# Performance work log

Hardware: AMD Instinct MI355X
Metric: run time of the kernel (lower is better)

Reference implementation:

```python
import jax, jax.numpy as jnp
import numpy as np

B, T_SEQ, STATE, DIM_IN, DIM_K, DIM_V, LAYER = 8, 2048, 128, 1024, 64, 64, 4
T = T_SEQ + 2 * STATE  # 2304
LAMBDA_INIT = 0.8 - 0.6 * float(np.exp(-0.3 * LAYER))
NEG = -1e30


def setup_inputs() -> dict:
    key = jax.random.key(0)
    ks = jax.random.split(key, 20)
    def w(k, shape):
        return jax.random.normal(k, shape, dtype=jnp.float32) * 0.02
    inp = {"x": jax.random.normal(ks[0], (B, T, DIM_IN), dtype=jnp.float32)}
    # projection weights stored as (in, out) so y = x @ W
    inp["Wq"] = w(ks[1], (DIM_IN, 2 * DIM_K)); inp["Wk"] = w(ks[2], (DIM_IN, 2 * DIM_K)); inp["Wv"] = w(ks[3], (DIM_IN, 2 * DIM_V))
    inp["Wq_ss"] = w(ks[4], (DIM_IN, 2 * DIM_K)); inp["Wk_ss"] = w(ks[5], (DIM_IN, 2 * DIM_K)); inp["Wv_ss"] = w(ks[6], (DIM_IN, 2 * DIM_V))
    inp["Wq_se"] = w(ks[7], (DIM_IN, 2 * DIM_K)); inp["Wk_se"] = w(ks[8], (DIM_IN, 2 * DIM_K)); inp["Wv_se"] = w(ks[9], (DIM_IN, 2 * DIM_V))
    # layernorm params (torch defaults: ones/zeros)
    inp["g_in"] = jnp.ones((DIM_IN,), jnp.float32); inp["b_in"] = jnp.zeros((DIM_IN,), jnp.float32)
    inp["g_ss"] = jnp.ones((DIM_IN,), jnp.float32); inp["b_ss"] = jnp.zeros((DIM_IN,), jnp.float32)
    inp["g_se"] = jnp.ones((DIM_IN,), jnp.float32); inp["b_se"] = jnp.zeros((DIM_IN,), jnp.float32)
    inp["g_out"] = jnp.ones((2 * DIM_V,), jnp.float32); inp["b_out"] = jnp.zeros((2 * DIM_V,), jnp.float32)
    # lambda gate params
    inp["lq1"] = jax.random.normal(ks[10], (1, DIM_K), jnp.float32)
    inp["lq2"] = jax.random.normal(ks[11], (1, DIM_K), jnp.float32)
    inp["lk1"] = jax.random.normal(ks[12], (DIM_K, 1), jnp.float32)
    inp["lk2"] = jax.random.normal(ks[13], (DIM_K, 1), jnp.float32)
    return inp


def _ln(z, g, b, eps=1e-5):
    m = jnp.mean(z, axis=-1, keepdims=True)
    v = jnp.mean((z - m) ** 2, axis=-1, keepdims=True)
    return (z - m) * jax.lax.rsqrt(v + eps) * g + b


def reference(x, Wq, Wk, Wv, Wq_ss, Wk_ss, Wv_ss, Wq_se, Wk_se, Wv_se,
              g_in, b_in, g_ss, b_ss, g_se, b_se, g_out, b_out,
              lq1, lq2, lk1, lk2):
    # extract_state: split off state tokens at both ends
    xs, xm, xe = x[:, :STATE], x[:, STATE:-STATE], x[:, -STATE:]
    xm = _ln(xm, g_in, b_in)
    xs = _ln(xs, g_ss, b_ss)
    xe = _ln(xe, g_se, b_se)
    q = jnp.concatenate([xs @ Wq_ss, xm @ Wq, xe @ Wq_se], axis=1)  # (B,T,2K)
    k = jnp.concatenate([xs @ Wk_ss, xm @ Wk, xe @ Wk_se], axis=1)
    v = jnp.concatenate([xs @ Wv_ss, xm @ Wv, xe @ Wv_se], axis=1)  # (B,T,2V)
    q1, q2 = q[..., :DIM_K], q[..., DIM_K:]
    k1, k2 = k[..., :DIM_K], k[..., DIM_K:]
    scale = 1.0 / np.sqrt(DIM_K)
    t = q.shape[1]
    causal = jnp.triu(jnp.full((t, t), NEG, dtype=q.dtype), k=1)  # (T,T)
    s1 = jnp.einsum('btd,bsd->bts', q1, k1) * scale + causal
    s2 = jnp.einsum('btd,bsd->bts', q2, k2) * scale + causal
    a1 = jax.nn.softmax(s1, axis=-1)
    a2 = jax.nn.softmax(s2, axis=-1)
    o1 = jnp.einsum('bts,bsd->btd', a1, v)
    o2 = jnp.einsum('bts,bsd->btd', a2, v)
    lam = (jnp.exp(lq1 @ lk1) - jnp.exp(lq2 @ lk2))[0, 0] + LAMBDA_INIT
    att = o1 - lam * o2
    return _ln(att, g_out, b_out)
```

## Files before the change

kernel.cpp:

```cpp
#include <hip/hip_runtime.h>
#include <hip/hip_bf16.h>
#include <stdint.h>

#define B_ 8
#define T_ 2304
#define DIN 1024
#define LAMBDA_INIT_F 0.6192834728526788f

typedef __bf16 bf16x8 __attribute__((ext_vector_type(8)));
typedef float f32x4 __attribute__((ext_vector_type(4)));

__device__ __forceinline__ unsigned short f2bf(float f) {
    union { float f; unsigned int u; } v; v.f = f;
    unsigned int u = v.u;
    unsigned int r = (u + 0x7FFFu + ((u >> 16) & 1u)) >> 16;
    return (unsigned short)r;
}

__device__ __forceinline__ unsigned int pack2bf(float lo, float hi) {
    return ((unsigned int)f2bf(hi) << 16) | (unsigned int)f2bf(lo);
}

__device__ __forceinline__ float bf2f(unsigned short u) {
    union { unsigned int u; float f; } v; v.u = ((unsigned int)u) << 16;
    return v.f;
}

__device__ __forceinline__ void gload16(const void* g, void* l) {
    __builtin_amdgcn_global_load_lds(
        (const __attribute__((address_space(1))) unsigned int*)g,
        (__attribute__((address_space(3))) unsigned int*)l,
        16, 0, 0);
}

__global__ __launch_bounds__(256) void k_wtrans(
    const float* w0, const float* w1, const float* w2,
    const float* w3, const float* w4, const float* w5,
    const float* w6, const float* w7, const float* w8,
    unsigned short* __restrict__ wt)
{
    __shared__ float tile[64][65];
    int bx = blockIdx.x;
    int mat = bx >> 5;
    int tl = bx & 31;
    int tx = tl & 15;
    int ty = tl >> 4;
    const float* srcs[9] = {w0, w1, w2, w3, w4, w5, w6, w7, w8};
    const float* src = srcs[mat];
    int k0 = tx * 64, c0 = ty * 64;
    int t = threadIdx.x;
    int r = t >> 2, cg = (t & 3) << 4;
    const float* p = src + (size_t)(k0 + r) * 128 + c0 + cg;
#pragma unroll
    for (int i = 0; i < 4; ++i) {
        float4 v = *(const float4*)(p + i * 4);
        tile[r][cg + i * 4 + 0] = v.x;
        tile[r][cg + i * 4 + 1] = v.y;
        tile[r][cg + i * 4 + 2] = v.z;
        tile[r][cg + i * 4 + 3] = v.w;
    }
    __syncthreads();
    int seg = mat / 3, m = mat % 3;
    int crow = seg * 384 + m * 128 + c0 + r;
    unsigned short* dst = wt + (size_t)crow * 1024 + k0 + cg;
    __align__(16) unsigned short ob[16];
#pragma unroll
    for (int i = 0; i < 16; ++i) ob[i] = f2bf(tile[cg + i][r]);
    *(uint4*)(dst) = *(const uint4*)(ob);
    *(uint4*)(dst + 8) = *(const uint4*)(ob + 8);
}

__global__ __launch_bounds__(256) void k_ln(
    const float* __restrict__ x,
    const float* __restrict__ g_in, const float* __restrict__ b_in,
    const float* __restrict__ g_ss, const float* __restrict__ b_ss,
    const float* __restrict__ g_se, const float* __restrict__ b_se,
    unsigned short* __restrict__ xbf)
{
    int row = (blockIdx.x << 2) + (threadIdx.x >> 6);
    int l = threadIdx.x & 63;
    int t = row % T_;
    const float* gv; const float* bv;
    if (t < 128)       { gv = g_ss; bv = b_ss; }
    else if (t < 2176) { gv = g_in; bv = b_in; }
    else               { gv = g_se; bv = b_se; }
    const float* xp = x + (size_t)row * DIN + l * 4;
    float4 v0 = *(const float4*)(xp);
    float4 v1 = *(const float4*)(xp + 256);
    float4 v2 = *(const float4*)(xp + 512);
    float4 v3 = *(const float4*)(xp + 768);
    float s  = v0.x + v0.y + v0.z + v0.w + v1.x + v1.y + v1.z + v1.w
             + v2.x + v2.y + v2.z + v2.w + v3.x + v3.y + v3.z + v3.w;
    float s2 = v0.x*v0.x + v0.y*v0.y + v0.z*v0.z + v0.w*v0.w
             + v1.x*v1.x + v1.y*v1.y + v1.z*v1.z + v1.w*v1.w
             + v2.x*v2.x + v2.y*v2.y + v2.z*v2.z + v2.w*v2.w
             + v3.x*v3.x + v3.y*v3.y + v3.z*v3.z + v3.w*v3.w;
#pragma unroll
    for (int off = 1; off <= 32; off <<= 1) {
        s  += __shfl_xor(s,  off);
        s2 += __shfl_xor(s2, off);
    }
    float mean = s * (1.f / 1024.f);
    float rstd = rsqrtf(s2 * (1.f / 1024.f) - mean * mean + 1e-5f);
    unsigned short* op = xbf + (size_t)row * DIN + l * 4;
    const float* gp = gv + l * 4;
    const float* bp = bv + l * 4;
#pragma unroll
    for (int k = 0; k < 4; ++k) {
        float4 vv = (k == 0) ? v0 : (k == 1) ? v1 : (k == 2) ? v2 : v3;
        float4 gk = *(const float4*)(gp + k * 256);
        float4 bk = *(const float4*)(bp + k * 256);
        uint2 o;
        o.x = pack2bf((vv.x - mean) * rstd * gk.x + bk.x,
                      (vv.y - mean) * rstd * gk.y + bk.y);
        o.y = pack2bf((vv.z - mean) * rstd * gk.z + bk.z,
                      (vv.w - mean) * rstd * gk.w + bk.w);
        *(uint2*)(op + k * 256) = o;
    }
}

__global__ __launch_bounds__(512, 4) void k_proj2(
    const unsigned short* __restrict__ xbf,
    const unsigned short* __restrict__ wt,
    unsigned short* __restrict__ qo,
    unsigned short* __restrict__ ko,
    unsigned short* __restrict__ vto)
{
    __shared__ __align__(16) char smem[81920];

    int bid = blockIdx.x;
    int mt = bid >> 1, ch = bid & 1;
    int bb = mt / 18, tt = mt % 18;
    int seg = (tt == 0) ? 0 : ((tt < 17) ? 1 : 2);
    size_t arow0 = (size_t)mt * 128;
    int ncol0 = ch * 192;
    int wrow0 = seg * 384 + ncol0;

    int tid = threadIdx.x;
    int w = tid >> 6, l = tid & 63;
    int wr = w >> 2, wc = w & 3;
    int g4 = l >> 4, cr = l & 15;

    int rA0 = tid >> 3, cS = (tid & 7) << 4;
    const char* srcA0 = (const char*)xbf + (arow0 + rA0) * 2048 + cS;
    const char* srcA1 = srcA0 + (size_t)64 * 2048;
    int dA0 = rA0 * 128 + (cS ^ ((rA0 & 7) << 4));
    int dA1 = dA0 + 64 * 128;
    const char* srcW0 = (const char*)wt + (size_t)(wrow0 + rA0) * 2048 + cS;
    const char* srcW1 = srcW0 + (size_t)64 * 2048;
    const char* srcW2 = srcW0 + (size_t)128 * 2048;
    int dW0 = dA0, dW1 = dA0 + 64 * 128, dW2 = dA0 + 128 * 128;

    {
        uint4 a0 = *(const uint4*)srcA0;
        uint4 a1 = *(const uint4*)srcA1;
        uint4 w0 = *(const uint4*)srcW0;
        uint4 w1 = *(const uint4*)srcW1;
        uint4 w2 = *(const uint4*)srcW2;
        *(uint4*)(smem + dA0) = a0;
        *(uint4*)(smem + dA1) = a1;
        *(uint4*)(smem + 32768 + dW0) = w0;
        *(uint4*)(smem + 32768 + dW1) = w1;
        *(uint4*)(smem + 32768 + dW2) = w2;
    }
    __syncthreads();

    f32x4 acc[4][3] = {};
    for (int ks = 0; ks < 16; ++ks) {
        bool pf = (ks < 15);
        uint4 pa0, pa1, pw0, pw1, pw2;
        if (pf) {
            size_t o = (size_t)(ks + 1) * 128;
            pa0 = *(const uint4*)(srcA0 + o);
            pa1 = *(const uint4*)(srcA1 + o);
            pw0 = *(const uint4*)(srcW0 + o);
            pw1 = *(const uint4*)(srcW1 + o);
            pw2 = *(const uint4*)(srcW2 + o);
        }
        const char* Ab = smem + (ks & 1) * 16384;
        const char* Wb = smem + 32768 + (ks & 1) * 24576;
        __builtin_amdgcn_s_setprio(1);
#pragma unroll
        for (int kk = 0; kk < 2; ++kk) {
            int kb = kk * 64 + g4 * 16;
            bf16x8 af[4];
#pragma unroll
            for (int r4 = 0; r4 < 4; ++r4) {
                int rr = wr * 64 + r4 * 16 + cr;
                af[r4] = *(const bf16x8*)(Ab + rr * 128 + (kb ^ ((rr & 7) << 4)));
            }
            bf16x8 bfr[3];
#pragma unroll
            for (int nt = 0; nt < 3; ++nt) {
                int c = wc * 48 + nt * 16 + cr;
                bfr[nt] = *(const bf16x8*)(Wb + c * 128 + (kb ^ ((c & 7) << 4)));
            }
#pragma unroll
            for (int r4 = 0; r4 < 4; ++r4)
#pragma unroll
                for (int nt = 0; nt < 3; ++nt)
                    acc[r4][nt] = __builtin_amdgcn_mfma_f32_16x16x32_bf16(af[r4], bfr[nt], acc[r4][nt], 0, 0, 0);
        }
        __builtin_amdgcn_s_setprio(0);
        __syncthreads();
        if (pf) {
            char* An = smem + ((ks + 1) & 1) * 16384;
            char* Wn = smem + 32768 + ((ks + 1) & 1) * 24576;
            *(uint4*)(An + dA0) = pa0;
            *(uint4*)(An + dA1) = pa1;
            *(uint4*)(Wn + dW0) = pw0;
            *(uint4*)(Wn + dW1) = pw1;
            *(uint4*)(Wn + dW2) = pw2;
        }
        __syncthreads();
    }

#pragma unroll
    for (int r4 = 0; r4 < 4; ++r4) {
        size_t grow = arow0 + wr * 64 + r4 * 16 + g4 * 4;
#pragma unroll
        for (int nt = 0; nt < 3; ++nt) {
            int c = ncol0 + wc * 48 + nt * 16 + cr;
            f32x4 a = acc[r4][nt];
            if (c < 128) {
#pragma unroll
                for (int g = 0; g < 4; ++g)
                    qo[(grow + g) * 128 + c] = f2bf(a[g]);
            } else if (c < 256) {
#pragma unroll
                for (int g = 0; g < 4; ++g)
                    ko[(grow + g) * 128 + (c - 128)] = f2bf(a[g]);
            } else {
                int cv = c - 256;
                int trow = tt * 128 + wr * 64 + r4 * 16 + g4 * 4;
                uint2 o;
                o.x = pack2bf(a[0], a[1]);
                o.y = pack2bf(a[2], a[3]);
                *(uint2*)(vto + ((size_t)bb * 128 + cv) * T_ + trow) = o;
            }
        }
    }
}

__global__ __launch_bounds__(256, 3) void k_attn(
    const unsigned short* __restrict__ qp_,
    const unsigned short* __restrict__ kp_,
    const unsigned short* __restrict__ vp_,
    const float* __restrict__ lq1, const float* __restrict__ lq2,
    const float* __restrict__ lk1, const float* __restrict__ lk2,
    const float* __restrict__ g_out, const float* __restrict__ b_out,
    unsigned short* __restrict__ opart,
    float* __restrict__ mlpart,
    float* __restrict__ out)
{
    __shared__ __align__(16) char smem[32768];

    int bid = blockIdx.x;
    int b = bid & 7;
    int u = 125 - (bid >> 3);
    int j, ci;
    if (u < 6) { j = u; ci = 0; }
    else {
        int v = u - 6;
        int g, base;
        if (v < 12)      { g = 0; base = 0;  }
        else if (v < 30) { g = 1; base = 12; }
        else if (v < 54) { g = 2; base = 30; }
        else if (v < 84) { g = 3; base = 54; }
        else             { g = 4; base = 84; }
        int w2 = v - base;
        int per = g + 2;
        int qd = w2 / per;
        j = 6 * (g + 1) + qd;
        ci = w2 - qd * per;
    }
    int nch = (j + 6) / 6;
    int c0 = ci * 6;
    int ntile = min(6, j + 1 - c0);
    int t0 = j * 64;

    int tid = threadIdx.x;
    int qg = tid >> 6;
    int l = tid & 63;
    int g4 = l >> 4, q = l & 15;
    int q_g = t0 + qg * 16 + q;

    int rbK = qg * 4 + (l >> 4);
    const char* kSrc0 = (const char*)kp_ + ((size_t)b * T_ + rbK) * 256
                      + (((l & 15) << 4) ^ ((rbK & 7) << 4));
    int rbV = qg * 8 + (l >> 3);
    const char* vSrc0 = (const char*)vp_ + ((size_t)b * 128 + rbV) * (T_ * 2)
                      + (((l & 7) << 4) ^ ((rbV & 7) << 4));
    char* ldsK = smem + qg * 1024;
    char* ldsV = smem + 16384 + qg * 1024;

    bf16x8 qf[2][2];
#pragma unroll
    for (int br = 0; br < 2; ++br)
#pragma unroll
        for (int h = 0; h < 2; ++h)
            qf[br][h] = *(const bf16x8*)(qp_ + ((size_t)b * T_ + q_g) * 128 + br * 64 + h * 32 + g4 * 8);

    {
        const char* kS = kSrc0 + (size_t)c0 * 16384;
        const char* vS = vSrc0 + (size_t)c0 * 128;
#pragma unroll
        for (int c = 0; c < 4; ++c) {
            gload16(kS + c * 4096, ldsK + c * 4096);
            gload16(vS + (size_t)c * 147456, ldsV + c * 4096);
        }
    }
    __syncthreads();

    float mrun[2] = {-1e30f, -1e30f};
    float lrun[2] = {0.f, 0.f};
    f32x4 oacc[2][8] = {};
    const char* Kb = smem;
    const char* Vb = smem + 16384;

    for (int t = 0; t < ntile; ++t) {
        int kt = c0 + t;
        bool diag = (kt == j);
        unsigned int pk[2][4][2];
#pragma unroll
        for (int br = 0; br < 2; ++br) {
            f32x4 s[4] = {};
            __builtin_amdgcn_s_setprio(1);
#pragma unroll
            for (int h = 0; h < 2; ++h) {
#pragma unroll
                for (int t4 = 0; t4 < 4; ++t4) {
                    int rk = t4 * 16 + q;
                    bf16x8 kf = *(const bf16x8*)(Kb + rk * 256 + ((br * 128 + h * 64 + g4 * 16) ^ ((rk & 7) << 4)));
                    s[t4] = __builtin_amdgcn_mfma_f32_16x16x32_bf16(kf, qf[br][h], s[t4], 0, 0, 0);
                }
            }
            __builtin_amdgcn_s_setprio(0);
            float sv[16];
            float mx = -1e30f;
#pragma unroll
            for (int t4 = 0; t4 < 4; ++t4)
#pragma unroll
                for (int r = 0; r < 4; ++r) {
                    float v = s[t4][r] * 0.125f;
                    if (diag) {
                        int kv_g = kt * 64 + t4 * 16 + g4 * 4 + r;
                        if (kv_g > q_g) v = -1e30f;
                    }
                    sv[t4 * 4 + r] = v;
                    mx = fmaxf(mx, v);
                }
            mx = fmaxf(mx, __shfl_xor(mx, 16));
            mx = fmaxf(mx, __shfl_xor(mx, 32));
            float mn;
            if (__all(mx <= mrun[br] + 8.f)) {
                mn = mrun[br];
            } else {
                mn = fmaxf(mrun[br], mx);
                float sf = __expf(mrun[br] - mn);
                mrun[br] = mn;
                lrun[br] *= sf;
#pragma unroll
                for (int dblk = 0; dblk < 8; ++dblk)
#pragma unroll
                    for (int r = 0; r < 4; ++r)
                        oacc[br][dblk][r] *= sf;
            }
            float pr[16];
            float rs = 0.f;
#pragma unroll
            for (int i = 0; i < 16; ++i) {
                pr[i] = __expf(sv[i] - mn);
                rs += pr[i];
            }
            rs += __shfl_xor(rs, 16);
            rs += __shfl_xor(rs, 32);
            lrun[br] += rs;
#pragma unroll
            for (int t4 = 0; t4 < 4; ++t4) {
                pk[br][t4][0] = pack2bf(pr[t4 * 4 + 0], pr[t4 * 4 + 1]);
                pk[br][t4][1] = pack2bf(pr[t4 * 4 + 2], pr[t4 * 4 + 3]);
            }
        }
#pragma unroll
        for (int h = 0; h < 2; ++h) {
            bf16x8 pb[2];
            int s0 = q + (((g4 * 2) & 3) << 4);
            int s1 = q + (((g4 * 2 + 1) & 3) << 4);
            int sel = g4 >> 1;
#pragma unroll
            for (int br = 0; br < 2; ++br) {
                unsigned int m0a = (unsigned int)__shfl((int)pk[br][0 + 2 * h][0], s0);
                unsigned int m0b = (unsigned int)__shfl((int)pk[br][1 + 2 * h][0], s0);
                unsigned int m1a = (unsigned int)__shfl((int)pk[br][0 + 2 * h][1], s0);
                unsigned int m1b = (unsigned int)__shfl((int)pk[br][1 + 2 * h][1], s0);
                unsigned int m2a = (unsigned int)__shfl((int)pk[br][0 + 2 * h][0], s1);
                unsigned int m2b = (unsigned int)__shfl((int)pk[br][1 + 2 * h][0], s1);
                unsigned int m3a = (unsigned int)__shfl((int)pk[br][0 + 2 * h][1], s1);
                unsigned int m3b = (unsigned int)__shfl((int)pk[br][1 + 2 * h][1], s1);
                union { unsigned int uv[4]; bf16x8 v; } pu;
                pu.uv[0] = sel ? m0b : m0a;
                pu.uv[1] = sel ? m1b : m1a;
                pu.uv[2] = sel ? m2b : m2a;
                pu.uv[3] = sel ? m3b : m3a;
                pb[br] = pu.v;
            }
            __builtin_amdgcn_s_setprio(1);
#pragma unroll
            for (int dblk = 0; dblk < 8; ++dblk) {
                int rv = dblk * 16 + q;
                bf16x8 vf = *(const bf16x8*)(Vb + rv * 128 + ((h * 64 + g4 * 16) ^ ((rv & 7) << 4)));
                oacc[0][dblk] = __builtin_amdgcn_mfma_f32_16x16x32_bf16(vf, pb[0], oacc[0][dblk], 0, 0, 0);
                oacc[1][dblk] = __builtin_amdgcn_mfma_f32_16x16x32_bf16(vf, pb[1], oacc[1][dblk], 0, 0, 0);
            }
            __builtin_amdgcn_s_setprio(0);
        }
        __syncthreads();
        if (t + 1 < ntile) {
            const char* kS = kSrc0 + (size_t)(kt + 1) * 16384;
            const char* vS = vSrc0 + (size_t)(kt + 1) * 128;
#pragma unroll
            for (int c = 0; c < 4; ++c) {
                gload16(kS + c * 4096, ldsK + c * 4096);
                gload16(vS + (size_t)c * 147456, ldsV + c * 4096);
            }
        }
        __syncthreads();
    }

    int row = qg * 16 + q;
    if (nch == 1) {
        float pa = lq1[l] * lk1[l];
        float pb2 = lq2[l] * lk2[l];
#pragma unroll
        for (int off = 32; off >= 1; off >>= 1) {
            pa += __shfl_xor(pa, off);
            pb2 += __shfl_xor(pb2, off);
        }
        float lam = __expf(pa) - __expf(pb2) + LAMBDA_INIT_F;

        float att[8][4];
        float sm = 0.f;
        float inv1 = 1.f / lrun[0], inv2 = 1.f / lrun[1];
#pragma unroll
        for (int dblk = 0; dblk < 8; ++dblk)
#pragma unroll
            for (int r = 0; r < 4; ++r) {
                float a = oacc[0][dblk][r] * inv1 - lam * (oacc[1][dblk][r] * inv2);
                att[dblk][r] = a;
                sm += a;
            }
        sm += __shfl_xor(sm, 16);
        sm += __shfl_xor(sm, 32);
        float mean = sm * (1.f / 128.f);
        float sv2 = 0.f;
#pragma unroll
        for (int dblk = 0; dblk < 8; ++dblk)
#pragma unroll
            for (int r = 0; r < 4; ++r) {
                float d = att[dblk][r] - mean;
                sv2 += d * d;
            }
        sv2 += __shfl_xor(sv2, 16);
        sv2 += __shfl_xor(sv2, 32);
        float rstd = rsqrtf(sv2 * (1.f / 128.f) + 1e-5f);

        float* orow = out + ((size_t)b * T_ + q_g) * 128;
#pragma unroll
        for (int dblk = 0; dblk < 8; ++dblk) {
            int d0 = dblk * 16 + g4 * 4;
            float4 o;
            o.x = (att[dblk][0] - mean) * rstd * g_out[d0 + 0] + b_out[d0 + 0];
            o.y = (att[dblk][1] - mean) * rstd * g_out[d0 + 1] + b_out[d0 + 1];
            o.z = (att[dblk][2] - mean) * rstd * g_out[d0 + 2] + b_out[d0 + 2];
            o.w = (att[dblk][3] - mean) * rstd * g_out[d0 + 3] + b_out[d0 + 3];
            *(float4*)(orow + d0) = o;
        }
    } else {
        int g2 = (j - 6) / 6;
        int off = 6 * g2 * (g2 + 3) / 2 + (j - 6 - 6 * g2) * (g2 + 2);
        int slot = b * 120 + off + ci;
        char* ob = (char*)opart + (size_t)slot * 32768;
#pragma unroll
        for (int br = 0; br < 2; ++br) {
#pragma unroll
            for (int dblk = 0; dblk < 8; ++dblk) {
                uint2 o;
                o.x = pack2bf(oacc[br][dblk][0], oacc[br][dblk][1]);
                o.y = pack2bf(oacc[br][dblk][2], oacc[br][dblk][3]);
                *(uint2*)(ob + br * 16384 + row * 256 + (dblk * 16 + g4 * 4) * 2) = o;
            }
            if (g4 == 0) {
                float2 mlv;
                mlv.x = mrun[br];
                mlv.y = lrun[br];
                *(float2*)(mlpart + ((size_t)slot * 128 + br * 64 + row) * 2) = mlv;
            }
        }
    }
}

__global__ __launch_bounds__(512) void k_merge(
    const unsigned short* __restrict__ opart,
    const float* __restrict__ mlpart,
    const float* __restrict__ lq1, const float* __restrict__ lq2,
    const float* __restrict__ lk1, const float* __restrict__ lk2,
    const float* __restrict__ g_out, const float* __restrict__ b_out,
    float* __restrict__ out)
{
    int bid = blockIdx.x;
    int b = bid & 7;
    int j = 6 + (bid >> 3);
    int nch = (j + 6) / 6;
    int g2 = (j - 6) / 6;
    int slotb = b * 120 + 6 * g2 * (g2 + 3) / 2 + (j - 6 - 6 * g2) * (g2 + 2);
    int tid = threadIdx.x;
    int row = tid >> 3;
    int d0 = (tid & 7) * 16;
    int l = tid & 63;

    float pa = lq1[l] * lk1[l];
    float pb = lq2[l] * lk2[l];
#pragma unroll
    for (int off = 32; off >= 1; off >>= 1) {
        pa += __shfl_xor(pa, off);
        pb += __shfl_xor(pb, off);
    }
    float lam = __expf(pa) - __expf(pb) + LAMBDA_INIT_F;

    float res[2][16];
#pragma unroll
    for (int br = 0; br < 2; ++br) {
        float mv0 = -1e30f, mv1 = -1e30f, mv2 = -1e30f,
              mv3 = -1e30f, mv4 = -1e30f, mv5 = -1e30f;
        float lv0 = 0.f, lv1 = 0.f, lv2 = 0.f, lv3 = 0.f, lv4 = 0.f, lv5 = 0.f;
        {
            const float* p0 = mlpart + ((size_t)slotb * 128 + br * 64 + row) * 2;
            mv0 = p0[0]; lv0 = p0[1];
            const float* p1 = mlpart + ((size_t)(slotb + 1) * 128 + br * 64 + row) * 2;
            mv1 = p1[0]; lv1 = p1[1];
            if (nch > 2) { const float* p = mlpart + ((size_t)(slotb + 2) * 128 + br * 64 + row) * 2; mv2 = p[0]; lv2 = p[1]; }
            if (nch > 3) { const float* p = mlpart + ((size_t)(slotb + 3) * 128 + br * 64 + row) * 2; mv3 = p[0]; lv3 = p[1]; }
            if (nch > 4) { const float* p = mlpart + ((size_t)(slotb + 4) * 128 + br * 64 + row) * 2; mv4 = p[0]; lv4 = p[1]; }
            if (nch > 5) { const float* p = mlpart + ((size_t)(slotb + 5) * 128 + br * 64 + row) * 2; mv5 = p[0]; lv5 = p[1]; }
        }
        float mstar = fmaxf(fmaxf(fmaxf(mv0, mv1), fmaxf(mv2, mv3)), fmaxf(mv4, mv5));
        float w0 = __expf(mv0 - mstar);
        float w1 = __expf(mv1 - mstar);
        float w2 = (nch > 2) ? __expf(mv2 - mstar) : 0.f;
        float w3 = (nch > 3) ? __expf(mv3 - mstar) : 0.f;
        float w4 = (nch > 4) ? __expf(mv4 - mstar) : 0.f;
        float w5 = (nch > 5) ? __expf(mv5 - mstar) : 0.f;
        float lsum = w0 * lv0 + w1 * lv1 + w2 * lv2 + w3 * lv3 + w4 * lv4 + w5 * lv5;

        float acc[16] = {};
#pragma unroll
        for (int c = 0; c < 6; ++c) {
            if (c >= nch) break;
            float wc = (c == 0) ? w0 : (c == 1) ? w1 : (c == 2) ? w2
                     : (c == 3) ? w3 : (c == 4) ? w4 : w5;
            const char* ob = (const char*)opart + (size_t)(slotb + c) * 32768
                           + br * 16384 + row * 256 + d0 * 2;
            uint4 v0 = *(const uint4*)(ob);
            uint4 v1 = *(const uint4*)(ob + 16);
            const unsigned int vv[8] = {v0.x, v0.y, v0.z, v0.w, v1.x, v1.y, v1.z, v1.w};
#pragma unroll
            for (int i = 0; i < 8; ++i) {
                acc[i * 2]     += wc * bf2f((unsigned short)(vv[i] & 0xFFFF));
                acc[i * 2 + 1] += wc * bf2f((unsigned short)(vv[i] >> 16));
            }
        }
        float inv = 1.f / lsum;
#pragma unroll
        for (int i = 0; i < 16; ++i) res[br][i] = acc[i] * inv;
    }

    float att[16];
    float sm = 0.f;
#pragma unroll
    for (int i = 0; i < 16; ++i) {
        att[i] = res[0][i] - lam * res[1][i];
        sm += att[i];
    }
    sm += __shfl_xor(sm, 1);
    sm += __shfl_xor(sm, 2);
    sm += __shfl_xor(sm, 4);
    float mean = sm * (1.f / 128.f);
    float sv2 = 0.f;
#pragma unroll
    for (int i = 0; i < 16; ++i) {
        float d = att[i] - mean;
        sv2 += d * d;
    }
    sv2 += __shfl_xor(sv2, 1);
    sv2 += __shfl_xor(sv2, 2);
    sv2 += __shfl_xor(sv2, 4);
    float rstd = rsqrtf(sv2 * (1.f / 128.f) + 1e-5f);

    float* orow = out + ((size_t)b * T_ + j * 64 + row) * 128 + d0;
#pragma unroll
    for (int k = 0; k < 4; ++k) {
        float4 o;
        o.x = (att[k * 4 + 0] - mean) * rstd * g_out[d0 + k * 4 + 0] + b_out[d0 + k * 4 + 0];
        o.y = (att[k * 4 + 1] - mean) * rstd * g_out[d0 + k * 4 + 1] + b_out[d0 + k * 4 + 1];
        o.z = (att[k * 4 + 2] - mean) * rstd * g_out[d0 + k * 4 + 2] + b_out[d0 + k * 4 + 2];
        o.w = (att[k * 4 + 3] - mean) * rstd * g_out[d0 + k * 4 + 3] + b_out[d0 + k * 4 + 3];
        *(float4*)(orow + k * 4) = o;
    }
}

extern "C" void kernel_launch(void* const* d_in, const int* in_sizes, int n_in,
                              void* d_out, int out_size, void* d_ws, size_t ws_size,
                              hipStream_t stream) {
    (void)in_sizes; (void)n_in; (void)out_size; (void)ws_size;
    const float* x = (const float*)d_in[0];
    char* ws = (char*)d_ws;
    unsigned short* wt  = (unsigned short*)ws;
    unsigned short* xbf = (unsigned short*)(ws + 2359296);
    unsigned short* qo  = (unsigned short*)(ws + 40108032);
    unsigned short* ko  = (unsigned short*)(ws + 44826624);
    unsigned short* vto = (unsigned short*)(ws + 49545216);
    unsigned short* opart = (unsigned short*)(ws + 2359296);
    float*          mlpart = (float*)(ws + 2359296 + 31457280);

    hipLaunchKernelGGL(k_wtrans, dim3(288), dim3(256), 0, stream,
        (const float*)d_in[4], (const float*)d_in[5], (const float*)d_in[6],
        (const float*)d_in[1], (const float*)d_in[2], (const float*)d_in[3],
        (const float*)d_in[7], (const float*)d_in[8], (const float*)d_in[9], wt);

    hipLaunchKernelGGL(k_ln, dim3(4608), dim3(256), 0, stream,
        x,
        (const float*)d_in[10], (const float*)d_in[11],
        (const float*)d_in[12], (const float*)d_in[13],
        (const float*)d_in[14], (const float*)d_in[15],
        xbf);

    hipLaunchKernelGGL(k_proj2, dim3(288), dim3(512), 0, stream,
        xbf, wt, qo, ko, vto);

    hipLaunchKernelGGL(k_attn, dim3(1008), dim3(256), 0, stream,
        qo, ko, vto,
        (const float*)d_in[18], (const float*)d_in[19],
        (const float*)d_in[20], (const float*)d_in[21],
        (const float*)d_in[16], (const float*)d_in[17],
        opart, mlpart,
        (float*)d_out);

    hipLaunchKernelGGL(k_merge, dim3(240), dim3(512), 0, stream,
        opart, mlpart,
        (const float*)d_in[18], (const float*)d_in[19],
        (const float*)d_in[20], (const float*)d_in[21],
        (const float*)d_in[16], (const float*)d_in[17],
        (float*)d_out);
}
```

Before: 118.5 us.

## Read K/V fragments directly from global memory instead of staging through LDS

The attention kernel no longer copies each 64-row K and V tile into shared memory with global_load_lds and two barriers per tile. Each wave now loads its MFMA K and V operands straight from global memory (relying on L1/L2 caching), which removes all block-level synchronization and LDS usage. The cost is that the four waves of a block each fetch the same K/V data separately, giving roughly four times the global/cache traffic and exposing load latency without explicit prefetch.

```diff
diff --git a/kernel.cpp b/kernel.cpp
--- a/kernel.cpp
+++ b/kernel.cpp
@@ -24,13 +24,6 @@
 __device__ __forceinline__ float bf2f(unsigned short u) {
     union { unsigned int u; float f; } v; v.u = ((unsigned int)u) << 16;
     return v.f;
-}
-
-__device__ __forceinline__ void gload16(const void* g, void* l) {
-    __builtin_amdgcn_global_load_lds(
-        (const __attribute__((address_space(1))) unsigned int*)g,
-        (__attribute__((address_space(3))) unsigned int*)l,
-        16, 0, 0);
 }
 
 __global__ __launch_bounds__(256) void k_wtrans(
@@ -253,8 +246,6 @@
     float* __restrict__ mlpart,
     float* __restrict__ out)
 {
-    __shared__ __align__(16) char smem[32768];
-
     int bid = blockIdx.x;
     int b = bid & 7;
     int u = 125 - (bid >> 3);
@@ -285,14 +276,8 @@
     int g4 = l >> 4, q = l & 15;
     int q_g = t0 + qg * 16 + q;
 
-    int rbK = qg * 4 + (l >> 4);
-    const char* kSrc0 = (const char*)kp_ + ((size_t)b * T_ + rbK) * 256
-                      + (((l & 15) << 4) ^ ((rbK & 7) << 4));
-    int rbV = qg * 8 + (l >> 3);
-    const char* vSrc0 = (const char*)vp_ + ((size_t)b * 128 + rbV) * (T_ * 2)
-                      + (((l & 7) << 4) ^ ((rbV & 7) << 4));
-    char* ldsK = smem + qg * 1024;
-    char* ldsV = smem + 16384 + qg * 1024;
+    const unsigned short* kfb = kp_ + ((size_t)b * T_ + q) * 128 + g4 * 8;
+    const unsigned short* vfb = vp_ + ((size_t)b * 128 + q) * T_ + g4 * 8;
 
     bf16x8 qf[2][2];
 #pragma unroll
@@ -300,27 +285,16 @@
 #pragma unroll
         for (int h = 0; h < 2; ++h)
             qf[br][h] = *(const bf16x8*)(qp_ + ((size_t)b * T_ + q_g) * 128 + br * 64 + h * 32 + g4 * 8);
-
-    {
-        const char* kS = kSrc0 + (size_t)c0 * 16384;
-        const char* vS = vSrc0 + (size_t)c0 * 128;
-#pragma unroll
-        for (int c = 0; c < 4; ++c) {
-            gload16(kS + c * 4096, ldsK + c * 4096);
-            gload16(vS + (size_t)c * 147456, ldsV + c * 4096);
-        }
-    }
-    __syncthreads();
 
     float mrun[2] = {-1e30f, -1e30f};
     float lrun[2] = {0.f, 0.f};
     f32x4 oacc[2][8] = {};
-    const char* Kb = smem;
-    const char* Vb = smem + 16384;
 
     for (int t = 0; t < ntile; ++t) {
         int kt = c0 + t;
         bool diag = (kt == j);
+        const unsigned short* kp = kfb + (size_t)kt * 64 * 128;
+        const unsigned short* vp = vfb + (size_t)kt * 64;
         unsigned int pk[2][4][2];
 #pragma unroll
         for (int br = 0; br < 2; ++br) {
@@ -330,8 +304,7 @@
             for (int h = 0; h < 2; ++h) {
 #pragma unroll
                 for (int t4 = 0; t4 < 4; ++t4) {
-                    int rk = t4 * 16 + q;
-                    bf16x8 kf = *(const bf16x8*)(Kb + rk * 256 + ((br * 128 + h * 64 + g4 * 16) ^ ((rk & 7) << 4)));
+                    bf16x8 kf = *(const bf16x8*)(kp + (size_t)t4 * 16 * 128 + br * 64 + h * 32);
                     s[t4] = __builtin_amdgcn_mfma_f32_16x16x32_bf16(kf, qf[br][h], s[t4], 0, 0, 0);
                 }
             }
@@ -408,24 +381,12 @@
             __builtin_amdgcn_s_setprio(1);
 #pragma unroll
             for (int dblk = 0; dblk < 8; ++dblk) {
-                int rv = dblk * 16 + q;
-                bf16x8 vf = *(const bf16x8*)(Vb + rv * 128 + ((h * 64 + g4 * 16) ^ ((rv & 7) << 4)));
+                bf16x8 vf = *(const bf16x8*)(vp + (size_t)dblk * 16 * T_ + h * 32);
                 oacc[0][dblk] = __builtin_amdgcn_mfma_f32_16x16x32_bf16(vf, pb[0], oacc[0][dblk], 0, 0, 0);
                 oacc[1][dblk] = __builtin_amdgcn_mfma_f32_16x16x32_bf16(vf, pb[1], oacc[1][dblk], 0, 0, 0);
             }
             __builtin_amdgcn_s_setprio(0);
         }
-        __syncthreads();
-        if (t + 1 < ntile) {
-            const char* kS = kSrc0 + (size_t)(kt + 1) * 16384;
-            const char* vS = vSrc0 + (size_t)(kt + 1) * 128;
-#pragma unroll
-            for (int c = 0; c < 4; ++c) {
-                gload16(kS + c * 4096, ldsK + c * 4096);
-                gload16(vS + (size_t)c * 147456, ldsV + c * 4096);
-            }
-        }
-        __syncthreads();
     }
 
     int row = qg * 16 + q;
```

Measured after the change: 196.4 us. 65.7% more time.
